# Optimization experiments

Measured on AMD Instinct MI355X. Metric: run time of the kernel, lower is better.

Reference implementation:

```python
import jax, jax.numpy as jnp
import numpy as np

N_EMBD = 1024
N_HEAD = 16

def setup_inputs() -> dict:
    key = jax.random.key(0)
    ks = jax.random.split(key, 8)
    C = N_EMBD
    s = 1.0 / np.sqrt(C)
    return {
        "x": jax.random.normal(ks[0], (8, 1024, C), jnp.float32),
        "encoder_output": jax.random.normal(ks[1], (8, 576, C), jnp.float32),
        "Wq": jax.random.normal(ks[2], (C, C), jnp.float32) * s,      # torch Linear weight [out,in]
        "bq": jnp.zeros((C,), jnp.float32),
        "Wkv": jax.random.normal(ks[3], (2 * C, C), jnp.float32) * s,
        "bkv": jnp.zeros((2 * C,), jnp.float32),
        "Wo": jax.random.normal(ks[4], (C, C), jnp.float32) * s,
        "bo": jnp.zeros((C,), jnp.float32),
    }

def reference(x, encoder_output, Wq, bq, Wkv, bkv, Wo, bo):
    B, T, C = x.shape
    I = encoder_output.shape[1]
    H, D = N_HEAD, C // N_HEAD
    q = jnp.einsum('btc,oc->bto', x, Wq) + bq                     # [B,T,C]
    kv = jnp.einsum('bic,oc->bio', encoder_output, Wkv) + bkv     # [B,I,2C]
    k, v = kv[..., :C], kv[..., C:]
    q = q.reshape(B, T, H, D).transpose(0, 2, 1, 3)               # [B,H,T,D]
    k = k.reshape(B, I, H, D).transpose(0, 2, 1, 3)               # [B,H,I,D]
    v = v.reshape(B, I, H, D).transpose(0, 2, 1, 3)               # [B,H,I,D]
    att = jnp.einsum('bhtd,bhid->bhti', q, k) * (1.0 / np.sqrt(D))
    att = jax.nn.softmax(att, axis=-1)                            # no mask: buffer unused in fwd
    y = jnp.einsum('bhti,bhid->bhtd', att, v)
    y = y.transpose(0, 2, 1, 3).reshape(B, T, C)
    return jnp.einsum('btc,oc->bto', y, Wo) + bo
```

## Files before the change

### kernel.cpp

```cpp
#include <hip/hip_runtime.h>
#include <type_traits>

typedef __bf16 bf16_t;
typedef __bf16 bfx8 __attribute__((ext_vector_type(8)));
typedef float  fx4  __attribute__((ext_vector_type(4)));

#define MFMA_BF16 __builtin_amdgcn_mfma_f32_16x16x32_bf16

#define BB 8
#define TT 1024
#define II 576
#define HH 16
#define DD 64
#define CC 1024

__device__ __forceinline__ void load_lds16(const void* g, void* l) {
    __builtin_amdgcn_global_load_lds(
        (const __attribute__((address_space(1))) void*)g,
        (__attribute__((address_space(3))) void*)l, 16, 0, 0);
}

__global__ __launch_bounds__(256)
void cvt_all(const float* __restrict__ x,  const float* __restrict__ enc,
             const float* __restrict__ wq, const float* __restrict__ wkv,
             const float* __restrict__ wo, const float* __restrict__ bq,
             const float* __restrict__ bkv,const float* __restrict__ bo,
             bf16_t* __restrict__ xb,  bf16_t* __restrict__ encb,
             bf16_t* __restrict__ wqb, bf16_t* __restrict__ wkvb,
             bf16_t* __restrict__ wob, bf16_t* __restrict__ bqb,
             bf16_t* __restrict__ bkvb,bf16_t* __restrict__ bob)
{
    const long total = 17305600;
    for (long e = ((long)blockIdx.x * 256 + threadIdx.x) * 8; e < total;
         e += (long)gridDim.x * 256 * 8) {
        const float* s; bf16_t* d; long off; float sc = 1.0f;
        if      (e <  8388608) { s = x;   d = xb;   off = e; }
        else if (e < 13107200) { s = enc; d = encb; off = e -  8388608; }
        else if (e < 14155776) { s = wq;  d = wqb;  off = e - 13107200; sc = 0.125f; }
        else if (e < 16252928) { s = wkv; d = wkvb; off = e - 14155776; }
        else if (e < 17301504) { s = wo;  d = wob;  off = e - 16252928; }
        else if (e < 17302528) { s = bq;  d = bqb;  off = e - 17301504; sc = 0.125f; }
        else if (e < 17304576) { s = bkv; d = bkvb; off = e - 17302528; }
        else                   { s = bo;  d = bob;  off = e - 17304576; }
        fx4 a = *reinterpret_cast<const fx4*>(s + off);
        fx4 b = *reinterpret_cast<const fx4*>(s + off + 4);
        bfx8 v;
#pragma unroll
        for (int i = 0; i < 4; i++) {
            v[i]     = (bf16_t)(a[i] * sc);
            v[4 + i] = (bf16_t)(b[i] * sc);
        }
        *reinterpret_cast<bfx8*>(d + off) = v;
    }
}


#define GEMM_STAGE(A_, W_, K_)                                                \
    {                                                                         \
        _Pragma("unroll")                                                     \
        for (int j = 0; j < 4; j++) {                                         \
            int e0  = (w * 4 + j) * 512;                                      \
            int row = (e0 >> 6) + (lane >> 3);                                \
            load_lds16(&A_[(long)(m0 + row) * K_ + k0 + colsw], &As[e0]);     \
        }                                                                     \
        _Pragma("unroll")                                                     \
        for (int j = 0; j < 2; j++) {                                         \
            int e0  = (w * 2 + j) * 512;                                      \
            int row = (e0 >> 6) + (lane >> 3);                                \
            load_lds16(&W_[(long)(n0 + row) * K_ + k0 + colsw], &Bs[e0]);     \
        }                                                                     \
    }

#define GEMM_MFMA()                                                           \
    _Pragma("unroll")                                                         \
    for (int kk = 0; kk < 2; kk++) {                                          \
        bfx8 af[4], bfr[2];                                                   \
        _Pragma("unroll")                                                     \
        for (int i = 0; i < 4; i++) {                                         \
            int R = wm + i * 16 + lrow;                                       \
            af[i] = *reinterpret_cast<const bfx8*>(                           \
                &As[R * 64 + (((kk * 4 + quad) ^ (lrow & 7)) * 8)]);          \
        }                                                                     \
        _Pragma("unroll")                                                     \
        for (int j = 0; j < 2; j++) {                                         \
            int R = wn + j * 16 + lrow;                                       \
            bfr[j] = *reinterpret_cast<const bfx8*>(                          \
                &Bs[R * 64 + (((kk * 4 + quad) ^ (lrow & 7)) * 8)]);          \
        }                                                                     \
        _Pragma("unroll")                                                     \
        for (int i = 0; i < 4; i++)                                           \
            _Pragma("unroll")                                                 \
            for (int j = 0; j < 2; j++)                                       \
                acc[i][j] = MFMA_BF16(af[i], bfr[j], acc[i][j], 0, 0, 0);     \
    }

__global__ __launch_bounds__(256)
void gemm_qkv(const bf16_t* __restrict__ xb,  const bf16_t* __restrict__ Wqb,
              const bf16_t* __restrict__ bqb, bf16_t* __restrict__ qout,
              const bf16_t* __restrict__ encb,const bf16_t* __restrict__ Wkvb,
              const bf16_t* __restrict__ bkvb,
              bf16_t* __restrict__ Kbuf, bf16_t* __restrict__ VTbuf)
{
    __shared__ __align__(16) bf16_t As[128 * 64];
    __shared__ __align__(16) bf16_t Bs[64 * 64];

    const int tid  = threadIdx.x;
    const int lane = tid & 63;
    const int w    = tid >> 6;
    const int wm   = (w >> 1) * 64;
    const int wn   = (w & 1) * 32;
    const int lrow = lane & 15;
    const int quad = lane >> 4;
    const int colsw = (((lane & 7) ^ ((lane >> 3) & 7)) * 8);

    int bid = blockIdx.x;
    const bf16_t *A, *W, *bias;
    int m0, n0, mode;
    if (bid < 1024) {
        mode = 0; A = xb; W = Wqb; bias = bqb;
        m0 = (bid >> 4) * 128; n0 = (bid & 15) * 64;
    } else {
        bid -= 1024;
        mode = 1; A = encb; W = Wkvb; bias = bkvb;
        m0 = (bid >> 5) * 128; n0 = (bid & 31) * 64;
    }
    const int K = 1024;

    fx4 acc[4][2];
#pragma unroll
    for (int i = 0; i < 4; i++)
#pragma unroll
        for (int j = 0; j < 2; j++) acc[i][j] = (fx4)0.0f;

    for (int k0 = 0; k0 < K; k0 += 64) {
        __syncthreads();
        GEMM_STAGE(A, W, K)
        __syncthreads();
        GEMM_MFMA()
    }

    if (mode == 0) {
#pragma unroll
        for (int i = 0; i < 4; i++)
#pragma unroll
            for (int j = 0; j < 2; j++) {
                int col  = n0 + wn + j * 16 + lrow;
                float bv = (float)bias[col];
                int row0 = m0 + wm + i * 16 + quad * 4;
#pragma unroll
                for (int r = 0; r < 4; r++)
                    qout[(long)(row0 + r) * 1024 + col] =
                        (bf16_t)(acc[i][j][r] + bv);
            }
    } else if (n0 < 1024) {
#pragma unroll
        for (int i = 0; i < 4; i++) {
            int row0 = m0 + wm + i * 16 + quad * 4;
#pragma unroll
            for (int r = 0; r < 4; r++) {
                unsigned m = row0 + r;
                unsigned b = m / 576u;
                unsigned ii = m - b * 576u;
#pragma unroll
                for (int j = 0; j < 2; j++) {
                    int col = n0 + wn + j * 16 + lrow;
                    int h = col >> 6, d = col & 63;
                    Kbuf[(((long)(b * 16 + h) * 576 + ii) << 6) + d] =
                        (bf16_t)(acc[i][j][r] + (float)bias[col]);
                }
            }
        }
    } else {
#pragma unroll
        for (int i = 0; i < 4; i++) {
            int row0 = m0 + wm + i * 16 + quad * 4;
#pragma unroll
            for (int r = 0; r < 4; r++) {
                unsigned m = row0 + r;
                unsigned b = m / 576u;
                unsigned ii = m - b * 576u;
#pragma unroll
                for (int j = 0; j < 2; j++) {
                    int col = n0 + wn + j * 16 + lrow;
                    int c2 = col - 1024;
                    int h = c2 >> 6, d = c2 & 63;
                    VTbuf[((long)(b * 16 + h) * 64 + d) * 576 + ii] =
                        (bf16_t)(acc[i][j][r] + (float)bias[col]);
                }
            }
        }
    }
}

template<typename TOUT>
__global__ __launch_bounds__(256)
void gemm2(const bf16_t* __restrict__ A, const bf16_t* __restrict__ W,
           const bf16_t* __restrict__ bias, TOUT* __restrict__ out,
           int M, int N, int K)
{
    __shared__ __align__(16) bf16_t As[128 * 64];
    __shared__ __align__(16) bf16_t Bs[64 * 64];

    const int tid  = threadIdx.x;
    const int lane = tid & 63;
    const int w    = tid >> 6;
    const int wm   = (w >> 1) * 64;
    const int wn   = (w & 1) * 32;
    const int lrow = lane & 15;
    const int quad = lane >> 4;
    const int colsw = (((lane & 7) ^ ((lane >> 3) & 7)) * 8);

    const int ntiles = N >> 6;
    const int m0 = (blockIdx.x / ntiles) * 128;
    const int n0 = (blockIdx.x % ntiles) * 64;

    fx4 acc[4][2];
#pragma unroll
    for (int i = 0; i < 4; i++)
#pragma unroll
        for (int j = 0; j < 2; j++) acc[i][j] = (fx4)0.0f;

    for (int k0 = 0; k0 < K; k0 += 64) {
        __syncthreads();
        GEMM_STAGE(A, W, K)
        __syncthreads();
        GEMM_MFMA()
    }

#pragma unroll
    for (int i = 0; i < 4; i++)
#pragma unroll
        for (int j = 0; j < 2; j++) {
            int col  = n0 + wn + j * 16 + lrow;
            float bv = (float)bias[col];
            int row0 = m0 + wm + i * 16 + quad * 4;
#pragma unroll
            for (int r = 0; r < 4; r++)
                out[(long)(row0 + r) * N + col] = (TOUT)(acc[i][j][r] + bv);
        }
}

__global__ __launch_bounds__(256)
void attn2(const bf16_t* __restrict__ q, const bf16_t* __restrict__ Kbuf,
           const bf16_t* __restrict__ VTbuf, bf16_t* __restrict__ y)
{
    __shared__ __align__(16) bf16_t Ks[64][72];
    __shared__ __align__(16) bf16_t Vt[64][72];
    __shared__ __align__(16) bf16_t Ps[4][32][72];

    const int tid  = threadIdx.x;
    const int lane = tid & 63;
    const int w    = tid >> 6;
    const int lrow = lane & 15;
    const int quad = lane >> 4;
    const int b  = blockIdx.z;
    const int h  = blockIdx.y;
    const int t0 = blockIdx.x * 128;

    const bf16_t* kb = Kbuf  + ((long)(b * 16 + h) * 576) * 64;
    const bf16_t* vb = VTbuf + ((long)(b * 16 + h) * 64) * 576;

    bfx8 qf[2][2];
#pragma unroll
    for (int mt = 0; mt < 2; mt++)
#pragma unroll
        for (int ks = 0; ks < 2; ks++)
            qf[mt][ks] = *reinterpret_cast<const bfx8*>(
                &q[(long)(b * TT + t0 + w * 32 + mt * 16 + lrow) * CC +
                   h * 64 + ks * 32 + quad * 8]);

    fx4 o[2][4];
    float lsum[2][4];
#pragma unroll
    for (int mt = 0; mt < 2; mt++)
#pragma unroll
        for (int dt = 0; dt < 4; dt++) o[mt][dt] = (fx4)0.0f;
#pragma unroll
    for (int mt = 0; mt < 2; mt++)
#pragma unroll
        for (int r = 0; r < 4; r++) lsum[mt][r] = 0.f;

    const int srow = tid >> 3;
    const int scol = (tid & 7) * 8;

    for (int ic = 0; ic < II / 64; ++ic) {
        __syncthreads();
#pragma unroll
        for (int it = 0; it < 2; it++) {
            int rr = srow + it * 32;
            *reinterpret_cast<bfx8*>(&Ks[rr][scol]) =
                *reinterpret_cast<const bfx8*>(&kb[(long)(ic * 64 + rr) * 64 + scol]);
            *reinterpret_cast<bfx8*>(&Vt[rr][scol]) =
                *reinterpret_cast<const bfx8*>(&vb[(long)rr * 576 + ic * 64 + scol]);
        }
        __syncthreads();

#pragma unroll
        for (int mt = 0; mt < 2; mt++) {
            fx4 s[4];
#pragma unroll
            for (int nt = 0; nt < 4; nt++) {
                s[nt] = (fx4)0.0f;
#pragma unroll
                for (int ks = 0; ks < 2; ks++) {
                    bfx8 bfr = *reinterpret_cast<const bfx8*>(
                        &Ks[nt * 16 + lrow][ks * 32 + quad * 8]);
                    s[nt] = MFMA_BF16(qf[mt][ks], bfr, s[nt], 0, 0, 0);
                }
            }
#pragma unroll
            for (int nt = 0; nt < 4; nt++)
#pragma unroll
                for (int r = 0; r < 4; r++) {
                    float p = __expf(s[nt][r]);
                    lsum[mt][r] += p;
                    Ps[w][mt * 16 + quad * 4 + r][nt * 16 + lrow] = (bf16_t)p;
                }
        }

        __asm__ __volatile__("s_waitcnt lgkmcnt(0)" ::: "memory");

#pragma unroll
        for (int mt = 0; mt < 2; mt++)
#pragma unroll
            for (int dt = 0; dt < 4; dt++)
#pragma unroll
                for (int ks = 0; ks < 2; ks++) {
                    bfx8 af = *reinterpret_cast<const bfx8*>(
                        &Ps[w][mt * 16 + lrow][ks * 32 + quad * 8]);
                    bfx8 bfr = *reinterpret_cast<const bfx8*>(
                        &Vt[dt * 16 + lrow][ks * 32 + quad * 8]);
                    o[mt][dt] = MFMA_BF16(af, bfr, o[mt][dt], 0, 0, 0);
                }
    }

#pragma unroll
    for (int mt = 0; mt < 2; mt++)
#pragma unroll
        for (int r = 0; r < 4; r++) {
            float l = lsum[mt][r];
#pragma unroll
            for (int off = 1; off < 16; off <<= 1)
                l += __shfl_xor(l, off, 64);
            float inv = 1.0f / l;
            int t = t0 + w * 32 + mt * 16 + quad * 4 + r;
#pragma unroll
            for (int dt = 0; dt < 4; dt++)
                y[(long)(b * TT + t) * CC + h * 64 + dt * 16 + lrow] =
                    (bf16_t)(o[mt][dt][r] * inv);
        }
}

template<typename TA, typename TOUT>
__global__ __launch_bounds__(256)
void gemm_bt_bias(const TA* __restrict__ A, const float* __restrict__ W,
                  const float* __restrict__ bias, TOUT* __restrict__ out,
                  int M, int N, int K, float escale)
{
    __shared__ __align__(16) bf16_t As[128][40];
    __shared__ __align__(16) bf16_t Bs[128][40];

    const int tid  = threadIdx.x;
    const int lane = tid & 63;
    const int wave = tid >> 6;
    const int wm   = (wave >> 1) * 64;
    const int wn   = (wave & 1) * 64;
    const int m0   = blockIdx.y * 128;
    const int n0   = blockIdx.x * 128;
    const int lrow = lane & 15;
    const int quad = lane >> 4;

    fx4 acc[4][4];
#pragma unroll
    for (int i = 0; i < 4; i++)
#pragma unroll
        for (int j = 0; j < 4; j++) acc[i][j] = (fx4)0.0f;

    for (int k0 = 0; k0 < K; k0 += 32) {
        __syncthreads();
#pragma unroll
        for (int r = 0; r < 2; ++r) {
            int idx = tid + r * 256;
            int row = idx >> 2;
            int col = (idx & 3) * 8;
            bfx8 av;
            if constexpr (std::is_same<TA, float>::value) {
                const float* sa = &A[(long)(m0 + row) * K + k0 + col];
                fx4 a0 = *reinterpret_cast<const fx4*>(sa);
                fx4 a1 = *reinterpret_cast<const fx4*>(sa + 4);
#pragma unroll
                for (int e = 0; e < 4; e++) { av[e] = (bf16_t)a0[e]; av[4+e] = (bf16_t)a1[e]; }
            } else {
                av = *reinterpret_cast<const bfx8*>(&A[(long)(m0 + row) * K + k0 + col]);
            }
            *reinterpret_cast<bfx8*>(&As[row][col]) = av;
            const float* sw = &W[(long)(n0 + row) * K + k0 + col];
            fx4 b0 = *reinterpret_cast<const fx4*>(sw);
            fx4 b1 = *reinterpret_cast<const fx4*>(sw + 4);
            bfx8 bv;
#pragma unroll
            for (int e = 0; e < 4; e++) { bv[e] = (bf16_t)b0[e]; bv[4+e] = (bf16_t)b1[e]; }
            *reinterpret_cast<bfx8*>(&Bs[row][col]) = bv;
        }
        __syncthreads();

        bfx8 af[4], bfr[4];
#pragma unroll
        for (int i = 0; i < 4; i++)
            af[i] = *reinterpret_cast<const bfx8*>(&As[wm + i * 16 + lrow][quad * 8]);
#pragma unroll
        for (int j = 0; j < 4; j++)
            bfr[j] = *reinterpret_cast<const bfx8*>(&Bs[wn + j * 16 + lrow][quad * 8]);
#pragma unroll
        for (int i = 0; i < 4; i++)
#pragma unroll
            for (int j = 0; j < 4; j++)
                acc[i][j] = MFMA_BF16(af[i], bfr[j], acc[i][j], 0, 0, 0);
    }

#pragma unroll
    for (int i = 0; i < 4; i++)
#pragma unroll
        for (int j = 0; j < 4; j++) {
            int col  = n0 + wn + j * 16 + lrow;
            float bv = bias[col];
            int row0 = m0 + wm + i * 16 + quad * 4;
#pragma unroll
            for (int r = 0; r < 4; r++)
                out[(long)(row0 + r) * N + col] = (TOUT)((acc[i][j][r] + bv) * escale);
        }
}

__global__ __launch_bounds__(256)
void attn_kernel(const bf16_t* __restrict__ q, const bf16_t* __restrict__ kv,
                 bf16_t* __restrict__ y, int b0)
{
    __shared__ __align__(16) bf16_t Ks[64][72];
    __shared__ __align__(16) bf16_t Vt[64][72];
    __shared__ __align__(16) bf16_t Ps[4][16][72];

    const int tid  = threadIdx.x;
    const int lane = tid & 63;
    const int w    = tid >> 6;
    const int lrow = lane & 15;
    const int quad = lane >> 4;
    const int bl = blockIdx.z;
    const int b  = b0 + bl;
    const int h  = blockIdx.y;
    const int t0 = blockIdx.x * 64;

    const int trow = t0 + w * 16 + lrow;
    bfx8 qf[2];
#pragma unroll
    for (int ks = 0; ks < 2; ++ks)
        qf[ks] = *reinterpret_cast<const bfx8*>(
            &q[(long)(b * TT + trow) * CC + h * 64 + ks * 32 + quad * 8]);

    float mrow[4], lsum[4];
    fx4 o[4];
#pragma unroll
    for (int r = 0; r < 4; r++) { mrow[r] = -1e30f; lsum[r] = 0.f; }
#pragma unroll
    for (int dt = 0; dt < 4; dt++) o[dt] = (fx4)0.0f;

    const int srow = tid >> 2;
    const int scol = (tid & 3) * 16;

    for (int ic = 0; ic < II / 64; ++ic) {
        __syncthreads();
        {
            long base = (long)(bl * II + ic * 64 + srow) * 2048 + h * 64 + scol;
            bfx8 k0v = *reinterpret_cast<const bfx8*>(&kv[base]);
            bfx8 k1v = *reinterpret_cast<const bfx8*>(&kv[base + 8]);
            *reinterpret_cast<bfx8*>(&Ks[srow][scol])     = k0v;
            *reinterpret_cast<bfx8*>(&Ks[srow][scol + 8]) = k1v;
            bfx8 v0 = *reinterpret_cast<const bfx8*>(&kv[base + 1024]);
            bfx8 v1 = *reinterpret_cast<const bfx8*>(&kv[base + 1032]);
#pragma unroll
            for (int e = 0; e < 8; e++) {
                Vt[scol + e][srow]     = v0[e];
                Vt[scol + 8 + e][srow] = v1[e];
            }
        }
        __syncthreads();

        fx4 s[4];
#pragma unroll
        for (int nt = 0; nt < 4; nt++) {
            s[nt] = (fx4)0.0f;
#pragma unroll
            for (int ks = 0; ks < 2; ks++) {
                bfx8 bfr = *reinterpret_cast<const bfx8*>(
                    &Ks[nt * 16 + lrow][ks * 32 + quad * 8]);
                s[nt] = MFMA_BF16(qf[ks], bfr, s[nt], 0, 0, 0);
            }
        }

        float p[4][4];
#pragma unroll
        for (int r = 0; r < 4; r++) {
            float mx = -1e30f;
#pragma unroll
            for (int nt = 0; nt < 4; nt++) mx = fmaxf(mx, s[nt][r]);
#pragma unroll
            for (int off = 1; off < 16; off <<= 1)
                mx = fmaxf(mx, __shfl_xor(mx, off, 64));
            float mnew  = fmaxf(mrow[r], mx);
            float alpha = __expf(mrow[r] - mnew);
            mrow[r] = mnew;
            float ps = 0.f;
#pragma unroll
            for (int nt = 0; nt < 4; nt++) {
                float pv = __expf(s[nt][r] - mnew);
                p[nt][r] = pv;
                ps += pv;
            }
#pragma unroll
            for (int off = 1; off < 16; off <<= 1)
                ps += __shfl_xor(ps, off, 64);
            lsum[r] = lsum[r] * alpha + ps;
#pragma unroll
            for (int dt = 0; dt < 4; dt++) o[dt][r] *= alpha;
        }

#pragma unroll
        for (int nt = 0; nt < 4; nt++)
#pragma unroll
            for (int r = 0; r < 4; r++)
                Ps[w][quad * 4 + r][nt * 16 + lrow] = (bf16_t)p[nt][r];

        __asm__ __volatile__("s_waitcnt lgkmcnt(0)" ::: "memory");

#pragma unroll
        for (int dt = 0; dt < 4; dt++)
#pragma unroll
            for (int ks = 0; ks < 2; ks++) {
                bfx8 af = *reinterpret_cast<const bfx8*>(
                    &Ps[w][lrow][ks * 32 + quad * 8]);
                bfx8 bfr = *reinterpret_cast<const bfx8*>(
                    &Vt[dt * 16 + lrow][ks * 32 + quad * 8]);
                o[dt] = MFMA_BF16(af, bfr, o[dt], 0, 0, 0);
            }
    }

#pragma unroll
    for (int dt = 0; dt < 4; dt++)
#pragma unroll
        for (int r = 0; r < 4; r++) {
            int t = t0 + w * 16 + quad * 4 + r;
            y[(long)(b * TT + t) * CC + h * 64 + dt * 16 + lrow] =
                (bf16_t)(o[dt][r] / lsum[r]);
        }
}

extern "C" void kernel_launch(void* const* d_in, const int* in_sizes, int n_in,
                              void* d_out, int out_size, void* d_ws, size_t ws_size,
                              hipStream_t stream)
{
    const float* x   = (const float*)d_in[0];
    const float* enc = (const float*)d_in[1];
    const float* Wq  = (const float*)d_in[2];
    const float* bq  = (const float*)d_in[3];
    const float* Wkv = (const float*)d_in[4];
    const float* bkv = (const float*)d_in[5];
    const float* Wo  = (const float*)d_in[6];
    const float* bo  = (const float*)d_in[7];
    float* out = (float*)d_out;

    bf16_t* qbuf = (bf16_t*)d_out;

    const size_t primary_need = 35131392ULL * 2;

    if (ws_size >= primary_need) {
        bf16_t* Kbuf  = (bf16_t*)d_ws;
        bf16_t* VTbuf = Kbuf  + (size_t)4718592;
        bf16_t* ybuf  = VTbuf + (size_t)4718592;
        bf16_t* xb    = ybuf  + (size_t)8388608;
        bf16_t* encb  = xb    + (size_t)8388608;
        bf16_t* Wqb   = encb  + (size_t)4718592;
        bf16_t* Wkvb  = Wqb   + (size_t)1048576;
        bf16_t* Wob   = Wkvb  + (size_t)2097152;
        bf16_t* bqb   = Wob   + (size_t)1048576;
        bf16_t* bkvb  = bqb   + 1024;
        bf16_t* bob   = bkvb  + 2048;

        cvt_all<<<4096, 256, 0, stream>>>(x, enc, Wq, Wkv, Wo, bq, bkv, bo,
                                          xb, encb, Wqb, Wkvb, Wob, bqb, bkvb, bob);
        gemm_qkv<<<2176, 256, 0, stream>>>(xb, Wqb, bqb, qbuf,
                                           encb, Wkvb, bkvb, Kbuf, VTbuf);
        attn2<<<dim3(8, 16, 8), 256, 0, stream>>>(qbuf, Kbuf, VTbuf, ybuf);
        gemm2<float><<<1024, 256, 0, stream>>>(ybuf, Wob, bob, out,
                                               8192, 1024, 1024);
    } else {
        bf16_t* kvbuf = (bf16_t*)d_ws;
        gemm_bt_bias<float, bf16_t><<<dim3(8, 64), 256, 0, stream>>>(
            x, Wq, bq, qbuf, 8192, 1024, 1024, 0.125f);
        const size_t full_need = ((size_t)4608 * 2048 + (size_t)8192 * 1024) * 2;
        if (ws_size >= full_need) {
            bf16_t* ybuf = kvbuf + (size_t)4608 * 2048;
            gemm_bt_bias<float, bf16_t><<<dim3(16, 36), 256, 0, stream>>>(
                enc, Wkv, bkv, kvbuf, 4608, 2048, 1024, 1.0f);
            attn_kernel<<<dim3(16, 16, 8), 256, 0, stream>>>(qbuf, kvbuf, ybuf, 0);
            gemm_bt_bias<bf16_t, float><<<dim3(8, 64), 256, 0, stream>>>(
                ybuf, Wo, bo, out, 8192, 1024, 1024, 1.0f);
        } else {
            bf16_t* ybuf = kvbuf + (size_t)1152 * 2048;
            for (int b0 = 0; b0 < BB; b0 += 2) {
                gemm_bt_bias<float, bf16_t><<<dim3(16, 9), 256, 0, stream>>>(
                    enc + (size_t)b0 * II * CC, Wkv, bkv, kvbuf, 1152, 2048, 1024, 1.0f);
                attn_kernel<<<dim3(16, 16, 2), 256, 0, stream>>>(qbuf, kvbuf, ybuf, b0);
            }
            gemm_bt_bias<bf16_t, float><<<dim3(8, 64), 256, 0, stream>>>(
                ybuf, Wo, bo, out, 8192, 1024, 1024, 1.0f);
        }
    }
}
```

Measured before the change: 241.3 us.

## Enlarge GEMM tiles to 128x128, hoist attention LDS fragment loads, flatten convert grid

Both GEMM kernels move from 128x64 to 128x128 output tiles, with each warp now computing a 64x64 sub-tile (4x4 MFMA accumulators). This raises arithmetic intensity per LDS load and halves the number of blocks. In the attention kernel, the K and V fragments are loaded from LDS once per tile and reused across both m-tiles, and the P fragments are hoisted out of the dt loop, which cuts redundant LDS reads. The convert kernel drops its grid-stride loop and launches one thread per 8 elements. The cost is more registers per thread (lower occupancy) and fewer GEMM blocks to spread across the CUs.

Result: no change. 245.3 us (+1.7%).

```diff
diff --git a/kernel.cpp b/kernel.cpp
--- a/kernel.cpp
+++ b/kernel.cpp
@@ -30,30 +30,26 @@
              bf16_t* __restrict__ wob, bf16_t* __restrict__ bqb,
              bf16_t* __restrict__ bkvb,bf16_t* __restrict__ bob)
 {
-    const long total = 17305600;
-    for (long e = ((long)blockIdx.x * 256 + threadIdx.x) * 8; e < total;
-         e += (long)gridDim.x * 256 * 8) {
-        const float* s; bf16_t* d; long off; float sc = 1.0f;
-        if      (e <  8388608) { s = x;   d = xb;   off = e; }
-        else if (e < 13107200) { s = enc; d = encb; off = e -  8388608; }
-        else if (e < 14155776) { s = wq;  d = wqb;  off = e - 13107200; sc = 0.125f; }
-        else if (e < 16252928) { s = wkv; d = wkvb; off = e - 14155776; }
-        else if (e < 17301504) { s = wo;  d = wob;  off = e - 16252928; }
-        else if (e < 17302528) { s = bq;  d = bqb;  off = e - 17301504; sc = 0.125f; }
-        else if (e < 17304576) { s = bkv; d = bkvb; off = e - 17302528; }
-        else                   { s = bo;  d = bob;  off = e - 17304576; }
-        fx4 a = *reinterpret_cast<const fx4*>(s + off);
-        fx4 b = *reinterpret_cast<const fx4*>(s + off + 4);
-        bfx8 v;
-#pragma unroll
-        for (int i = 0; i < 4; i++) {
-            v[i]     = (bf16_t)(a[i] * sc);
-            v[4 + i] = (bf16_t)(b[i] * sc);
-        }
-        *reinterpret_cast<bfx8*>(d + off) = v;
-    }
-}
-
+    long e = ((long)blockIdx.x * 256 + threadIdx.x) * 8;
+    const float* s; bf16_t* d; long off; float sc = 1.0f;
+    if      (e <  8388608) { s = x;   d = xb;   off = e; }
+    else if (e < 13107200) { s = enc; d = encb; off = e -  8388608; }
+    else if (e < 14155776) { s = wq;  d = wqb;  off = e - 13107200; sc = 0.125f; }
+    else if (e < 16252928) { s = wkv; d = wkvb; off = e - 14155776; }
+    else if (e < 17301504) { s = wo;  d = wob;  off = e - 16252928; }
+    else if (e < 17302528) { s = bq;  d = bqb;  off = e - 17301504; sc = 0.125f; }
+    else if (e < 17304576) { s = bkv; d = bkvb; off = e - 17302528; }
+    else                   { s = bo;  d = bob;  off = e - 17304576; }
+    fx4 a = *reinterpret_cast<const fx4*>(s + off);
+    fx4 b = *reinterpret_cast<const fx4*>(s + off + 4);
+    bfx8 v;
+#pragma unroll
+    for (int i = 0; i < 4; i++) {
+        v[i]     = (bf16_t)(a[i] * sc);
+        v[4 + i] = (bf16_t)(b[i] * sc);
+    }
+    *reinterpret_cast<bfx8*>(d + off) = v;
+}
 
 #define GEMM_STAGE(A_, W_, K_)                                                \
     {                                                                         \
@@ -64,8 +60,8 @@
             load_lds16(&A_[(long)(m0 + row) * K_ + k0 + colsw], &As[e0]);     \
         }                                                                     \
         _Pragma("unroll")                                                     \
-        for (int j = 0; j < 2; j++) {                                         \
-            int e0  = (w * 2 + j) * 512;                                      \
+        for (int j = 0; j < 4; j++) {                                         \
+            int e0  = (w * 4 + j) * 512;                                      \
             int row = (e0 >> 6) + (lane >> 3);                                \
             load_lds16(&W_[(long)(n0 + row) * K_ + k0 + colsw], &Bs[e0]);     \
         }                                                                     \
@@ -74,7 +70,7 @@
 #define GEMM_MFMA()                                                           \
     _Pragma("unroll")                                                         \
     for (int kk = 0; kk < 2; kk++) {                                          \
-        bfx8 af[4], bfr[2];                                                   \
+        bfx8 af[4], bfr[4];                                                   \
         _Pragma("unroll")                                                     \
         for (int i = 0; i < 4; i++) {                                         \
             int R = wm + i * 16 + lrow;                                       \
@@ -82,7 +78,7 @@
                 &As[R * 64 + (((kk * 4 + quad) ^ (lrow & 7)) * 8)]);          \
         }                                                                     \
         _Pragma("unroll")                                                     \
-        for (int j = 0; j < 2; j++) {                                         \
+        for (int j = 0; j < 4; j++) {                                         \
             int R = wn + j * 16 + lrow;                                       \
             bfr[j] = *reinterpret_cast<const bfx8*>(                          \
                 &Bs[R * 64 + (((kk * 4 + quad) ^ (lrow & 7)) * 8)]);          \
@@ -90,7 +86,7 @@
         _Pragma("unroll")                                                     \
         for (int i = 0; i < 4; i++)                                           \
             _Pragma("unroll")                                                 \
-            for (int j = 0; j < 2; j++)                                       \
+            for (int j = 0; j < 4; j++)                                       \
                 acc[i][j] = MFMA_BF16(af[i], bfr[j], acc[i][j], 0, 0, 0);     \
     }
 
@@ -102,13 +98,13 @@
               bf16_t* __restrict__ Kbuf, bf16_t* __restrict__ VTbuf)
 {
     __shared__ __align__(16) bf16_t As[128 * 64];
-    __shared__ __align__(16) bf16_t Bs[64 * 64];
+    __shared__ __align__(16) bf16_t Bs[128 * 64];
 
     const int tid  = threadIdx.x;
     const int lane = tid & 63;
     const int w    = tid >> 6;
     const int wm   = (w >> 1) * 64;
-    const int wn   = (w & 1) * 32;
+    const int wn   = (w & 1) * 64;
     const int lrow = lane & 15;
     const int quad = lane >> 4;
     const int colsw = (((lane & 7) ^ ((lane >> 3) & 7)) * 8);
@@ -116,21 +112,21 @@
     int bid = blockIdx.x;
     const bf16_t *A, *W, *bias;
     int m0, n0, mode;
-    if (bid < 1024) {
+    if (bid < 512) {
         mode = 0; A = xb; W = Wqb; bias = bqb;
-        m0 = (bid >> 4) * 128; n0 = (bid & 15) * 64;
+        m0 = (bid >> 3) * 128; n0 = (bid & 7) * 128;
     } else {
-        bid -= 1024;
+        bid -= 512;
         mode = 1; A = encb; W = Wkvb; bias = bkvb;
-        m0 = (bid >> 5) * 128; n0 = (bid & 31) * 64;
+        m0 = (bid >> 4) * 128; n0 = (bid & 15) * 128;
     }
     const int K = 1024;
 
-    fx4 acc[4][2];
+    fx4 acc[4][4];
 #pragma unroll
     for (int i = 0; i < 4; i++)
 #pragma unroll
-        for (int j = 0; j < 2; j++) acc[i][j] = (fx4)0.0f;
+        for (int j = 0; j < 4; j++) acc[i][j] = (fx4)0.0f;
 
     for (int k0 = 0; k0 < K; k0 += 64) {
         __syncthreads();
@@ -143,7 +139,7 @@
 #pragma unroll
         for (int i = 0; i < 4; i++)
 #pragma unroll
-            for (int j = 0; j < 2; j++) {
+            for (int j = 0; j < 4; j++) {
                 int col  = n0 + wn + j * 16 + lrow;
                 float bv = (float)bias[col];
                 int row0 = m0 + wm + i * 16 + quad * 4;
@@ -162,7 +158,7 @@
                 unsigned b = m / 576u;
                 unsigned ii = m - b * 576u;
 #pragma unroll
-                for (int j = 0; j < 2; j++) {
+                for (int j = 0; j < 4; j++) {
                     int col = n0 + wn + j * 16 + lrow;
                     int h = col >> 6, d = col & 63;
                     Kbuf[(((long)(b * 16 + h) * 576 + ii) << 6) + d] =
@@ -180,7 +176,7 @@
                 unsigned b = m / 576u;
                 unsigned ii = m - b * 576u;
 #pragma unroll
-                for (int j = 0; j < 2; j++) {
+                for (int j = 0; j < 4; j++) {
                     int col = n0 + wn + j * 16 + lrow;
                     int c2 = col - 1024;
                     int h = c2 >> 6, d = c2 & 63;
@@ -199,26 +195,26 @@
            int M, int N, int K)
 {
     __shared__ __align__(16) bf16_t As[128 * 64];
-    __shared__ __align__(16) bf16_t Bs[64 * 64];
+    __shared__ __align__(16) bf16_t Bs[128 * 64];
 
     const int tid  = threadIdx.x;
     const int lane = tid & 63;
     const int w    = tid >> 6;
     const int wm   = (w >> 1) * 64;
-    const int wn   = (w & 1) * 32;
+    const int wn   = (w & 1) * 64;
     const int lrow = lane & 15;
     const int quad = lane >> 4;
     const int colsw = (((lane & 7) ^ ((lane >> 3) & 7)) * 8);
 
-    const int ntiles = N >> 6;
+    const int ntiles = N >> 7;
     const int m0 = (blockIdx.x / ntiles) * 128;
-    const int n0 = (blockIdx.x % ntiles) * 64;
-
-    fx4 acc[4][2];
+    const int n0 = (blockIdx.x % ntiles) * 128;
+
+    fx4 acc[4][4];
 #pragma unroll
     for (int i = 0; i < 4; i++)
 #pragma unroll
-        for (int j = 0; j < 2; j++) acc[i][j] = (fx4)0.0f;
+        for (int j = 0; j < 4; j++) acc[i][j] = (fx4)0.0f;
 
     for (int k0 = 0; k0 < K; k0 += 64) {
         __syncthreads();
@@ -230,7 +226,7 @@
 #pragma unroll
     for (int i = 0; i < 4; i++)
 #pragma unroll
-        for (int j = 0; j < 2; j++) {
+        for (int j = 0; j < 4; j++) {
             int col  = n0 + wn + j * 16 + lrow;
             float bv = (float)bias[col];
             int row0 = m0 + wm + i * 16 + quad * 4;
@@ -295,6 +291,14 @@
         }
         __syncthreads();
 
+        bfx8 kf[4][2];
+#pragma unroll
+        for (int nt = 0; nt < 4; nt++)
+#pragma unroll
+            for (int ks = 0; ks < 2; ks++)
+                kf[nt][ks] = *reinterpret_cast<const bfx8*>(
+                    &Ks[nt * 16 + lrow][ks * 32 + quad * 8]);
+
 #pragma unroll
         for (int mt = 0; mt < 2; mt++) {
             fx4 s[4];
@@ -302,11 +306,8 @@
             for (int nt = 0; nt < 4; nt++) {
                 s[nt] = (fx4)0.0f;
 #pragma unroll
-                for (int ks = 0; ks < 2; ks++) {
-                    bfx8 bfr = *reinterpret_cast<const bfx8*>(
-                        &Ks[nt * 16 + lrow][ks * 32 + quad * 8]);
-                    s[nt] = MFMA_BF16(qf[mt][ks], bfr, s[nt], 0, 0, 0);
-                }
+                for (int ks = 0; ks < 2; ks++)
+                    s[nt] = MFMA_BF16(qf[mt][ks], kf[nt][ks], s[nt], 0, 0, 0);
             }
 #pragma unroll
             for (int nt = 0; nt < 4; nt++)
@@ -320,18 +321,27 @@
 
         __asm__ __volatile__("s_waitcnt lgkmcnt(0)" ::: "memory");
 
-#pragma unroll
-        for (int mt = 0; mt < 2; mt++)
+        bfx8 vf[4][2];
+#pragma unroll
+        for (int dt = 0; dt < 4; dt++)
+#pragma unroll
+            for (int ks = 0; ks < 2; ks++)
+                vf[dt][ks] = *reinterpret_cast<const bfx8*>(
+                    &Vt[dt * 16 + lrow][ks * 32 + quad * 8]);
+
+#pragma unroll
+        for (int mt = 0; mt < 2; mt++) {
+            bfx8 af[2];
+#pragma unroll
+            for (int ks = 0; ks < 2; ks++)
+                af[ks] = *reinterpret_cast<const bfx8*>(
+                    &Ps[w][mt * 16 + lrow][ks * 32 + quad * 8]);
 #pragma unroll
             for (int dt = 0; dt < 4; dt++)
 #pragma unroll
-                for (int ks = 0; ks < 2; ks++) {
-                    bfx8 af = *reinterpret_cast<const bfx8*>(
-                        &Ps[w][mt * 16 + lrow][ks * 32 + quad * 8]);
-                    bfx8 bfr = *reinterpret_cast<const bfx8*>(
-                        &Vt[dt * 16 + lrow][ks * 32 + quad * 8]);
-                    o[mt][dt] = MFMA_BF16(af, bfr, o[mt][dt], 0, 0, 0);
-                }
+                for (int ks = 0; ks < 2; ks++)
+                    o[mt][dt] = MFMA_BF16(af[ks], vf[dt][ks], o[mt][dt], 0, 0, 0);
+        }
     }
 
 #pragma unroll
@@ -584,13 +594,13 @@
         bf16_t* bkvb  = bqb   + 1024;
         bf16_t* bob   = bkvb  + 2048;
 
-        cvt_all<<<4096, 256, 0, stream>>>(x, enc, Wq, Wkv, Wo, bq, bkv, bo,
+        cvt_all<<<8450, 256, 0, stream>>>(x, enc, Wq, Wkv, Wo, bq, bkv, bo,
                                           xb, encb, Wqb, Wkvb, Wob, bqb, bkvb, bob);
-        gemm_qkv<<<2176, 256, 0, stream>>>(xb, Wqb, bqb, qbuf,
+        gemm_qkv<<<1088, 256, 0, stream>>>(xb, Wqb, bqb, qbuf,
                                            encb, Wkvb, bkvb, Kbuf, VTbuf);
         attn2<<<dim3(8, 16, 8), 256, 0, stream>>>(qbuf, Kbuf, VTbuf, ybuf);
-        gemm2<float><<<1024, 256, 0, stream>>>(ybuf, Wob, bob, out,
-                                               8192, 1024, 1024);
+        gemm2<float><<<512, 256, 0, stream>>>(ybuf, Wob, bob, out,
+                                              8192, 1024, 1024);
     } else {
         bf16_t* kvbuf = (bf16_t*)d_ws;
         gemm_bt_bias<float, bf16_t><<<dim3(8, 64), 256, 0, stream>>>(
```
